# Kernel optimization log

Hardware: AMD Instinct MI355X
Metric: run time of the kernel (lower is better)

## Reference

```python
import jax, jax.numpy as jnp
import numpy as np

D = 1024; DI = 2048; HS = 16; PS = DI // HS; NS = 64; KC = 4; CHUNK = 64
HA = 16; HKV = 4; PA = D // HA; MLP_MULT = 4; ROPE_BASE = 10000.0
B_SZ = 2; L_SEQ = 2048


def rms_norm(x):
    eps = jnp.asarray(jnp.finfo(x.dtype).eps, x.dtype)
    return x * jax.lax.rsqrt(jnp.mean(jnp.square(x), axis=-1, keepdims=True) + eps)


def silu(x):
    return x * jax.nn.sigmoid(x)


def apply_rope(x, cos, sin):
    half = x.shape[-1] // 2
    x1, x2 = x[..., :half], x[..., half:]
    return jnp.concatenate([x1 * cos + x2 * sin, -x1 * sin + x2 * cos], axis=-1)


def selective_scan(x, A, Bm, Cm, dt, chunk):
    # x: [B,L,H,P], Bm/Cm: [B,L,H,N], A/dt: [H]. L must be a multiple of chunk.
    Bb, L, H, P = x.shape
    N = Bm.shape[-1]
    decay = jnp.exp(A * dt)  # [H]
    nc = L // chunk
    xp = x.reshape(Bb, nc, chunk, H, P).transpose(0, 1, 3, 2, 4)   # [B,nc,H,cs,P]
    Bp = Bm.reshape(Bb, nc, chunk, H, N).transpose(0, 1, 3, 2, 4)  # [B,nc,H,cs,N]
    Cp = Cm.reshape(Bb, nc, chunk, H, N).transpose(0, 1, 3, 2, 4)
    x_dt = xp * dt[None, None, :, None, None]
    idx = jnp.arange(chunk)
    diff = idx[:, None] - idx[None, :]
    # intra-chunk causal decay matrix L_mat: [H,cs,cs]
    Lm = jnp.where(diff >= 0, decay[:, None, None] ** jnp.maximum(diff, 0), 0.0)
    CB = jnp.einsum('bchqn,bchkn->bchqk', Cp, Bp)
    y_diag = jnp.einsum('bchqk,bchkp->bchqp', CB * Lm[None, None], x_dt)
    # per-chunk states
    decay_rev = decay[:, None] ** (chunk - 1 - idx)[None, :]  # [H,cs]
    states = jnp.einsum('bchtn,bchtp->bchnp', Bp * decay_rev[None, None, :, :, None], x_dt)
    # inter-chunk propagation
    ci = jnp.arange(nc)
    shift = ci[:, None] - ci[None, :] - 1
    cdec = decay ** chunk
    M = jnp.where(shift >= 0, cdec[:, None, None] ** jnp.maximum(shift, 0), 0.0)  # [H,nc,nc]
    h_carry = jnp.einsum('hij,bjhnp->bihnp', M, states)
    decay_out = decay[:, None] ** (idx + 1)[None, :]  # [H,cs]
    y_off = jnp.einsum('bchtn,bchnp->bchtp', Cp, h_carry) * decay_out[None, None, :, :, None]
    y = (y_diag + y_off).transpose(0, 1, 3, 2, 4).reshape(Bb, L, H, P)
    return y


def mlp(n, fc_w, proj_w):
    h = jax.nn.relu(n @ fc_w)
    return jnp.square(h) @ proj_w


def setup_inputs() -> dict:
    key = jax.random.key(0)
    ks = jax.random.split(key, 24)
    w = lambda k, shp, s=0.02: jax.random.normal(k, shp, jnp.float32) * s
    dt_init = jax.random.uniform(ks[0], (HS,), jnp.float32, 0.001, 0.1)
    dt_bias = dt_init + jnp.log(-jnp.expm1(-dt_init))  # inverse softplus
    return {
        'x': jax.random.normal(ks[1], (B_SZ, L_SEQ, D), jnp.float32),
        'in_proj_w': w(ks[2], (D, 2 * DI)),
        'conv_w': w(ks[3], (DI, KC), 0.2),
        'conv_b': jnp.zeros((DI,), jnp.float32),
        'B_proj_w': w(ks[4], (D, HS * NS)),
        'C_proj_w': w(ks[5], (D, HS * NS)),
        'dt_bias': dt_bias,
        'A_log': jnp.log(jnp.arange(1, HS + 1, dtype=jnp.float32)),
        'D_param': jnp.ones((HS,), jnp.float32),
        'out_proj_w': w(ks[6], (DI, D)),
        'resid_mix_m': jnp.stack([jnp.ones(D), jnp.zeros(D)]).astype(jnp.float32),
        'mamba_scale': jnp.ones((D,), jnp.float32),
        'm_fc_w': w(ks[7], (D, MLP_MULT * D)),
        'm_proj_w': w(ks[8], (MLP_MULT * D, D)),
        'm_mlp_scale': jnp.ones((D,), jnp.float32),
        'resid_mix_a': jnp.stack([jnp.ones(D), jnp.zeros(D)]).astype(jnp.float32),
        'q_w': w(ks[9], (D, D)),
        'k_w': w(ks[10], (D, HKV * PA)),
        'v_w': w(ks[11], (D, HKV * PA)),
        'o_w': w(ks[12], (D, D)),
        'q_gain': jnp.full((HA,), 1.0, jnp.float32),
        'attn_scale': jnp.ones((D,), jnp.float32),
        'a_fc_w': w(ks[13], (D, MLP_MULT * D)),
        'a_proj_w': w(ks[14], (MLP_MULT * D, D)),
        'a_mlp_scale': jnp.ones((D,), jnp.float32),
    }


def reference(x, in_proj_w, conv_w, conv_b, B_proj_w, C_proj_w, dt_bias, A_log, D_param, out_proj_w, resid_mix_m, mamba_scale, m_fc_w, m_proj_w, m_mlp_scale, resid_mix_a, q_w, k_w, v_w, o_w, q_gain, attn_scale, a_fc_w, a_proj_w, a_mlp_scale):
    Bb, L, _ = x.shape
    x0 = x
    # ---- Mamba block ----
    xm = resid_mix_m[0][None, None] * x + resid_mix_m[1][None, None] * x0
    n = rms_norm(xm)
    vg = n @ in_proj_w
    value, gate = vg[..., :DI], vg[..., DI:]
    v_t = value.transpose(0, 2, 1)  # [B, DI, L]
    v_conv = jax.lax.conv_general_dilated(
        v_t, conv_w[:, None, :], (1,), [(KC - 1, 0)],
        feature_group_count=DI, dimension_numbers=('NCH', 'OIH', 'NCH')) + conv_b[None, :, None]
    value = silu(v_conv).transpose(0, 2, 1).reshape(Bb, L, HS, PS)
    Bm = (xm @ B_proj_w).reshape(Bb, L, HS, NS)  # B/C use pre-norm (mixed) input
    Cm = (xm @ C_proj_w).reshape(Bb, L, HS, NS)
    dt = jax.nn.softplus(dt_bias)
    A = -jnp.exp(A_log)
    y = selective_scan(value, A, Bm, Cm, dt, CHUNK)
    y = y + D_param[None, None, :, None] * value
    y = (y.reshape(Bb, L, DI) * silu(gate)) @ out_proj_w
    xm = xm + mamba_scale[None, None] * y
    xm = xm + m_mlp_scale[None, None] * mlp(rms_norm(xm), m_fc_w, m_proj_w)
    # ---- Attention block ----
    xa = resid_mix_a[0][None, None] * xm + resid_mix_a[1][None, None] * x0
    n = rms_norm(xa)
    q = (n @ q_w).reshape(Bb, L, HA, PA).transpose(0, 2, 1, 3)
    k = (n @ k_w).reshape(Bb, L, HKV, PA).transpose(0, 2, 1, 3)
    v = (n @ v_w).reshape(Bb, L, HKV, PA).transpose(0, 2, 1, 3)
    q = rms_norm(q); k = rms_norm(k)
    inv_freq = 1.0 / (ROPE_BASE ** (jnp.arange(0, PA, 2, dtype=jnp.float32) / PA))
    f = jnp.outer(jnp.arange(L, dtype=jnp.float32), inv_freq)
    cos, sin = jnp.cos(f)[None, None], jnp.sin(f)[None, None]
    q = apply_rope(q, cos, sin) * q_gain[None, :, None, None]
    k = apply_rope(k, cos, sin)
    G = HA // HKV
    k = jnp.repeat(k, G, axis=1); v = jnp.repeat(v, G, axis=1)
    s = jnp.einsum('bhqd,bhkd->bhqk', q, k) / np.float32(np.sqrt(PA))
    mask = jnp.tril(jnp.ones((L, L), bool))
    s = jnp.where(mask[None, None], s, jnp.asarray(-jnp.inf, s.dtype))
    att = jax.nn.softmax(s, axis=-1)
    y = jnp.einsum('bhqk,bhkd->bhqd', att, v).transpose(0, 2, 1, 3).reshape(Bb, L, D)
    xa = xa + attn_scale[None, None] * (y @ o_w)
    xa = xa + a_mlp_scale[None, None] * mlp(rms_norm(xa), a_fc_w, a_proj_w)
    return xa
```

## Files before the change

kernel.cpp:

```cpp
#include <hip/hip_runtime.h>
#include <hip/hip_bf16.h>
#include <math.h>

#define D_ 1024
#define DI_ 2048
#define HS_ 16
#define PS_ 128
#define NS_ 64
#define HA_ 16
#define HKV_ 4
#define PA_ 64
#define B_ 2
#define L_ 2048
#define NT_ 4096
#define NC_ 32
#define RMS_EPS_ 1.1920929e-7f

typedef __attribute__((ext_vector_type(8))) short short8;
typedef __attribute__((ext_vector_type(4))) float f32x4;

#define GLOAD_LDS16(gp, lp)                                                        \
  __builtin_amdgcn_global_load_lds(                                               \
      (const __attribute__((address_space(1))) unsigned int*)(gp),                \
      (__attribute__((address_space(3))) unsigned int*)(lp), 16, 0, 0)

__global__ __launch_bounds__(256) void transpose_cvt(
    const float* __restrict__ W, __hip_bfloat16* __restrict__ Wt, int K, int N, int ldw) {
  __shared__ float t[32][33];
  int n0 = blockIdx.x * 32, k0 = blockIdx.y * 32;
  int tx = threadIdx.x & 31, ty = threadIdx.x >> 5;
#pragma unroll
  for (int i = 0; i < 4; i++)
    t[ty + i * 8][tx] = W[(size_t)(k0 + ty + i * 8) * ldw + n0 + tx];
  __syncthreads();
#pragma unroll
  for (int i = 0; i < 4; i++)
    Wt[(size_t)(n0 + ty + i * 8) * K + k0 + tx] = __float2bfloat16(t[tx][ty + i * 8]);
}

template<int BN>
__global__ __launch_bounds__(256) void gemm_bf16_t(
    const unsigned short* __restrict__ A, const unsigned short* __restrict__ Wt,
    float* __restrict__ Cf, __hip_bfloat16* __restrict__ Cb,
    const float* __restrict__ baseb, const float* __restrict__ scale,
    int N, int K, int mode) {
  constexpr int nWc = BN / 64;
  constexpr int nWr = 4 / nWc;
  constexpr int MF  = 8 / nWr;
  __shared__ unsigned short As[2][128 * 64];
  __shared__ unsigned short Bs[2][BN * 64];
  int bm = blockIdx.y * 128, bn = blockIdx.x * BN;
  int tid = threadIdx.x;
  int w = tid >> 6, l = tid & 63;
  int wr = w / nWc, wc = w % nWc;
  int l15 = l & 15, lg = l >> 4;
  f32x4 acc[MF][4];
#pragma unroll
  for (int i = 0; i < MF; i++)
#pragma unroll
    for (int j = 0; j < 4; j++) acc[i][j] = (f32x4){0.f, 0.f, 0.f, 0.f};
  int r_ = tid >> 3;
  int s_ = tid & 7;

  auto STAGE = [&](int k0, int nb) {
#pragma unroll
    for (int i = 0; i < 4; i++) {
      int r = i * 32 + r_;
      int kq = s_ ^ (r & 7);
      GLOAD_LDS16(A + (size_t)(bm + r) * K + k0 + kq * 8, &As[nb][r * 64 + s_ * 8]);
    }
#pragma unroll
    for (int i = 0; i < BN / 32; i++) {
      int r = i * 32 + r_;
      int kq = s_ ^ (r & 7);
      GLOAD_LDS16(Wt + (size_t)(bn + r) * K + k0 + kq * 8, &Bs[nb][r * 64 + s_ * 8]);
    }
  };

  STAGE(0, 0);
  __syncthreads();
  int cur = 0;
  for (int k0 = 0; k0 < K; k0 += 64) {
    if (k0 + 64 < K) STAGE(k0 + 64, cur ^ 1);
#pragma unroll
    for (int h = 0; h < 2; h++) {
      short8 af[MF], bfr[4];
#pragma unroll
      for (int i = 0; i < MF; i++) {
        int row = wr * (16 * MF) + i * 16 + l15;
        int c = h * 4 + lg;
        af[i] = *(const short8*)&As[cur][row * 64 + ((c ^ (row & 7)) << 3)];
      }
#pragma unroll
      for (int j = 0; j < 4; j++) {
        int row = wc * 64 + j * 16 + l15;
        int c = h * 4 + lg;
        bfr[j] = *(const short8*)&Bs[cur][row * 64 + ((c ^ (row & 7)) << 3)];
      }
#pragma unroll
      for (int i = 0; i < MF; i++)
#pragma unroll
        for (int j = 0; j < 4; j++)
          acc[i][j] = __builtin_amdgcn_mfma_f32_16x16x32_bf16(af[i], bfr[j], acc[i][j], 0, 0, 0);
    }
    __syncthreads();
    cur ^= 1;
  }
  int rb = lg * 4, cb2 = l15;
#pragma unroll
  for (int i = 0; i < MF; i++)
#pragma unroll
    for (int j = 0; j < 4; j++) {
      int gr = bm + wr * (16 * MF) + i * 16 + rb;
      int gc = bn + wc * 64 + j * 16 + cb2;
#pragma unroll
      for (int reg = 0; reg < 4; reg++) {
        float v = acc[i][j][reg];
        size_t idx = (size_t)(gr + reg) * N + gc;
        if (mode == 0) {
          Cf[idx] = v;
        } else if (mode == 1) {
          v = fmaxf(v, 0.f);
          Cb[idx] = __float2bfloat16(v * v);
        } else if (mode == 2) {
          Cb[idx] = __float2bfloat16(v);
        } else {
          Cf[idx] = baseb[idx] + scale[gc] * v;
        }
      }
    }
}

__global__ __launch_bounds__(256) void mix_rms_kernel(
    const float* __restrict__ a, const float* __restrict__ b2,
    const float* __restrict__ mix, float* __restrict__ xout,
    __hip_bfloat16* __restrict__ nbf, __hip_bfloat16* __restrict__ rawbf) {
  int row = blockIdx.x;
  size_t base = (size_t)row * D_;
  float v[4]; float ss = 0.f;
#pragma unroll
  for (int i = 0; i < 4; i++) {
    int d = threadIdx.x + i * 256;
    float val = mix[d] * a[base + d] + mix[D_ + d] * b2[base + d];
    v[i] = val; ss += val * val;
  }
  for (int o = 32; o > 0; o >>= 1) ss += __shfl_down(ss, o, 64);
  __shared__ float red[4];
  if ((threadIdx.x & 63) == 0) red[threadIdx.x >> 6] = ss;
  __syncthreads();
  float inv = rsqrtf((red[0] + red[1] + red[2] + red[3]) * (1.f / D_) + RMS_EPS_);
#pragma unroll
  for (int i = 0; i < 4; i++) {
    int d = threadIdx.x + i * 256;
    xout[base + d] = v[i];
    nbf[base + d] = __float2bfloat16(v[i] * inv);
    if (rawbf) rawbf[base + d] = __float2bfloat16(v[i]);
  }
}

__global__ __launch_bounds__(256) void rms_kernel(
    const float* __restrict__ a, __hip_bfloat16* __restrict__ nbf) {
  int row = blockIdx.x;
  size_t base = (size_t)row * D_;
  float v[4]; float ss = 0.f;
#pragma unroll
  for (int i = 0; i < 4; i++) {
    int d = threadIdx.x + i * 256;
    float val = a[base + d];
    v[i] = val; ss += val * val;
  }
  for (int o = 32; o > 0; o >>= 1) ss += __shfl_down(ss, o, 64);
  __shared__ float red[4];
  if ((threadIdx.x & 63) == 0) red[threadIdx.x >> 6] = ss;
  __syncthreads();
  float inv = rsqrtf((red[0] + red[1] + red[2] + red[3]) * (1.f / D_) + RMS_EPS_);
#pragma unroll
  for (int i = 0; i < 4; i++) {
    int d = threadIdx.x + i * 256;
    nbf[base + d] = __float2bfloat16(v[i] * inv);
  }
}

__global__ __launch_bounds__(256) void conv_silu_kernel(
    const __hip_bfloat16* __restrict__ vg, const float* __restrict__ cw,
    const float* __restrict__ cb, float* __restrict__ xv) {
  int idx = blockIdx.x * 256 + threadIdx.x;
  int c = idx & (DI_ - 1);
  int bl = idx >> 11;
  int l = bl & (L_ - 1);
  float acc = cb[c];
  float w0 = cw[c * 4 + 0], w1 = cw[c * 4 + 1], w2 = cw[c * 4 + 2], w3 = cw[c * 4 + 3];
  size_t rb = (size_t)bl * 4096 + c;
  if (l >= 3) acc += __bfloat162float(vg[rb - (size_t)3 * 4096]) * w0;
  if (l >= 2) acc += __bfloat162float(vg[rb - (size_t)2 * 4096]) * w1;
  if (l >= 1) acc += __bfloat162float(vg[rb - (size_t)1 * 4096]) * w2;
  acc += __bfloat162float(vg[rb]) * w3;
  xv[idx] = acc / (1.f + __expf(-acc));
}

__global__ __launch_bounds__(256) void scanA1_kernel(
    const float* __restrict__ xv, const __hip_bfloat16* __restrict__ BCm,
    const float* __restrict__ dt_bias, const float* __restrict__ A_log,
    float* __restrict__ st) {
  __shared__ __align__(16) float sm[4096 + 8192];
  float* Bs = sm;
  float* Xs = sm + 4096;
  int blk = blockIdx.x;
  int c = blk & 31, h = (blk >> 5) & 15, b = blk >> 9;
  float dt = log1pf(__expf(dt_bias[h]));
  float adt = -__expf(A_log[h]) * dt;
  int tid = threadIdx.x;
  int l0 = c * 64;
  size_t rB = ((size_t)(b * L_ + l0)) * 2048 + h * NS_;
#pragma unroll
  for (int i = 0; i < 16; i++) {
    int e = tid + i * 256;
    int t = e >> 6, n = e & 63;
    Bs[t * 64 + n] = __bfloat162float(BCm[rB + (size_t)t * 2048 + n]);
  }
  size_t rX = ((size_t)(b * L_ + l0)) * DI_ + h * PS_;
#pragma unroll
  for (int i = 0; i < 32; i++) {
    int e = tid + i * 256;
    int t = e >> 7, p = e & 127;
    Xs[t * 128 + p] = xv[rX + (size_t)t * DI_ + p];
  }
  __syncthreads();
  int pg = tid & 31;
  int ng = (tid >> 5) << 3;
  float acc[8][4];
#pragma unroll
  for (int nn = 0; nn < 8; nn++)
#pragma unroll
    for (int i = 0; i < 4; i++) acc[nn][i] = 0.f;
  for (int t = 0; t < 64; t++) {
    float dr = __expf(adt * (float)(63 - t));
    float4 x4 = *(const float4*)&Xs[t * 128 + pg * 4];
    float xd0 = x4.x * dr, xd1 = x4.y * dr, xd2 = x4.z * dr, xd3 = x4.w * dr;
#pragma unroll
    for (int nn = 0; nn < 8; nn++) {
      float bv = Bs[t * 64 + ng + nn];
      acc[nn][0] += bv * xd0; acc[nn][1] += bv * xd1;
      acc[nn][2] += bv * xd2; acc[nn][3] += bv * xd3;
    }
  }
  size_t sb = ((size_t)((b * HS_ + h) * NC_ + c)) * (NS_ * PS_);
#pragma unroll
  for (int nn = 0; nn < 8; nn++) {
    *(float4*)&st[sb + (size_t)(ng + nn) * PS_ + pg * 4] =
        make_float4(acc[nn][0] * dt, acc[nn][1] * dt, acc[nn][2] * dt, acc[nn][3] * dt);
  }
}

__global__ __launch_bounds__(256) void scanA2_kernel(
    const float* __restrict__ xv, const __hip_bfloat16* __restrict__ BCm,
    const float* __restrict__ dt_bias,
    const float* __restrict__ A_log, const float* __restrict__ D_param,
    float* __restrict__ y) {
  __shared__ __align__(16) float sm[4160 + 8192];
  float* Cb = sm;
  float* Bs = sm + 4160;
  float* Xs = sm + 4160;
  int blk = blockIdx.x;
  int c = blk & 31, h = (blk >> 5) & 15, b = blk >> 9;
  float dt = log1pf(__expf(dt_bias[h]));
  float adt = -__expf(A_log[h]) * dt;
  float Dp = D_param[h];
  int tid = threadIdx.x;
  int l0 = c * 64;
  size_t rB = ((size_t)(b * L_ + l0)) * 2048 + h * NS_;
#pragma unroll
  for (int i = 0; i < 16; i++) {
    int e = tid + i * 256;
    int t = e >> 6, n = e & 63;
    Bs[t * 64 + n] = __bfloat162float(BCm[rB + (size_t)t * 2048 + n]);
    Cb[t * 65 + n] = __bfloat162float(BCm[rB + 1024 + (size_t)t * 2048 + n]);
  }
  __syncthreads();
  int q = tid >> 2;
  int kb = (tid & 3) << 4;
  float cbl[16];
#pragma unroll
  for (int kk = 0; kk < 16; kk++) {
    int k = kb + kk;
    float a = 0.f;
    if (k <= q) {
      for (int n = 0; n < 64; n++) a += Cb[q * 65 + n] * Bs[k * 64 + n];
      a *= __expf(adt * (float)(q - k));
    }
    cbl[kk] = a;
  }
  __syncthreads();
#pragma unroll
  for (int kk = 0; kk < 16; kk++) Cb[q * 65 + kb + kk] = cbl[kk];
  size_t rX = ((size_t)(b * L_ + l0)) * DI_ + h * PS_;
#pragma unroll
  for (int i = 0; i < 32; i++) {
    int e = tid + i * 256;
    int t = e >> 7, p = e & 127;
    Xs[t * 128 + p] = xv[rX + (size_t)t * DI_ + p];
  }
  __syncthreads();
  int pg = tid & 31;
  int qg = (tid >> 5) << 3;
  float acc[8][4];
#pragma unroll
  for (int qq = 0; qq < 8; qq++)
#pragma unroll
    for (int i = 0; i < 4; i++) acc[qq][i] = 0.f;
  for (int k = 0; k < 64; k++) {
    float4 x4 = *(const float4*)&Xs[k * 128 + pg * 4];
#pragma unroll
    for (int qq = 0; qq < 8; qq++) {
      float s = Cb[(qg + qq) * 65 + k];
      acc[qq][0] += s * x4.x; acc[qq][1] += s * x4.y;
      acc[qq][2] += s * x4.z; acc[qq][3] += s * x4.w;
    }
  }
#pragma unroll
  for (int qq = 0; qq < 8; qq++) {
    int qr = qg + qq;
    float4 xq = *(const float4*)&Xs[qr * 128 + pg * 4];
    size_t yo = ((size_t)(b * L_ + l0 + qr)) * DI_ + h * PS_ + pg * 4;
    *(float4*)&y[yo] = make_float4(acc[qq][0] * dt + Dp * xq.x,
                                   acc[qq][1] * dt + Dp * xq.y,
                                   acc[qq][2] * dt + Dp * xq.z,
                                   acc[qq][3] * dt + Dp * xq.w);
  }
}

__global__ __launch_bounds__(256) void scanB1_kernel(
    float* __restrict__ st, const float* __restrict__ dt_bias,
    const float* __restrict__ A_log) {
  int slice = blockIdx.x & 3;
  int h = (blockIdx.x >> 2) & 15, b = blockIdx.x >> 6;
  float dt = log1pf(__expf(dt_bias[h]));
  float adt = -__expf(A_log[h]) * dt;
  float cdec = __expf(adt * 64.f);
  size_t base = ((size_t)(b * HS_ + h)) * NC_ * (NS_ * PS_) + slice * 2048 + threadIdx.x;
  float hreg[8];
#pragma unroll
  for (int j = 0; j < 8; j++) hreg[j] = 0.f;
  for (int c = 0; c < NC_; c++) {
    size_t o = base + (size_t)c * (NS_ * PS_);
#pragma unroll
    for (int j = 0; j < 8; j++) {
      float tmp = st[o + (size_t)j * 256];
      st[o + (size_t)j * 256] = hreg[j];
      hreg[j] = cdec * hreg[j] + tmp;
    }
  }
}

__global__ __launch_bounds__(256) void scanB2_kernel(
    const __hip_bfloat16* __restrict__ BCm, const float* __restrict__ st,
    const __hip_bfloat16* __restrict__ vg, const float* __restrict__ dt_bias,
    const float* __restrict__ A_log, const float* __restrict__ y,
    __hip_bfloat16* __restrict__ yout) {
  __shared__ float Cs[64 * 64];
  __shared__ __align__(16) float Hs[64 * 128];
  int blk = blockIdx.x;
  int c = blk & 31, h = (blk >> 5) & 15, b = blk >> 9;
  float dt = log1pf(__expf(dt_bias[h]));
  float adt = -__expf(A_log[h]) * dt;
  int tid = threadIdx.x;
  int l0 = c * 64;
  size_t rC = ((size_t)(b * L_ + l0)) * 2048 + 1024 + h * NS_;
#pragma unroll
  for (int i = 0; i < 16; i++) {
    int e = tid + i * 256;
    int t = e >> 6, n = e & 63;
    Cs[t * 64 + n] = __bfloat162float(BCm[rC + (size_t)t * 2048 + n]);
  }
  size_t sb = ((size_t)((b * HS_ + h) * NC_ + c)) * (NS_ * PS_);
#pragma unroll
  for (int i = 0; i < 32; i++) {
    int e = tid + i * 256;
    Hs[e] = st[sb + e];
  }
  __syncthreads();
  int pg = tid & 31;
  int tg = (tid >> 5) << 3;
  float acc[8][4];
#pragma unroll
  for (int tt = 0; tt < 8; tt++)
#pragma unroll
    for (int i = 0; i < 4; i++) acc[tt][i] = 0.f;
  for (int n = 0; n < 64; n++) {
    float4 h4 = *(const float4*)&Hs[n * 128 + pg * 4];
#pragma unroll
    for (int tt = 0; tt < 8; tt++) {
      float cv = Cs[(tg + tt) * 64 + n];
      acc[tt][0] += cv * h4.x; acc[tt][1] += cv * h4.y;
      acc[tt][2] += cv * h4.z; acc[tt][3] += cv * h4.w;
    }
  }
#pragma unroll
  for (int tt = 0; tt < 8; tt++) {
    int t = tg + tt;
    float dout = __expf(adt * (float)(t + 1));
    size_t row = (size_t)(b * L_ + l0 + t);
#pragma unroll
    for (int i = 0; i < 4; i++) {
      int p = pg * 4 + i;
      float g = __bfloat162float(vg[row * 4096 + 2048 + h * PS_ + p]);
      float yv = y[row * DI_ + h * PS_ + p] + acc[tt][i] * dout;
      yout[row * DI_ + h * PS_ + p] = __float2bfloat16(yv * (g / (1.f + __expf(-g))));
    }
  }
}

__global__ void rope_fill_kernel(float* __restrict__ cosb, float* __restrict__ sinb) {
  int idx = blockIdx.x * 256 + threadIdx.x;
  int i = idx & 31, l = idx >> 5;
  float inv = __expf(-(2.0f * (float)i / (float)PA_) * logf(10000.0f));
  float ang = (float)l * inv;
  cosb[idx] = cosf(ang);
  sinb[idx] = sinf(ang);
}

__global__ __launch_bounds__(256) void qknorm_rope_bf16_kernel(
    const float* __restrict__ src, int srcstride, int srcofs,
    __hip_bfloat16* __restrict__ dst, int nh,
    const float* __restrict__ cosb, const float* __restrict__ sinb,
    const float* __restrict__ gain) {
  int row = blockIdx.x * 4 + (threadIdx.x >> 6);
  int lane = threadIdx.x & 63;
  int h = row % nh;
  int tok = row / nh;
  int l = tok & (L_ - 1);
  float v = src[(size_t)tok * srcstride + srcofs + h * 64 + lane];
  float ss = v * v;
  for (int o = 32; o > 0; o >>= 1) ss += __shfl_xor(ss, o, 64);
  v *= rsqrtf(ss * (1.f / PA_) + RMS_EPS_);
  float partner = __shfl_xor(v, 32, 64);
  int i = lane & 31;
  float cth = cosb[l * 32 + i], sth = sinb[l * 32 + i];
  float out = (lane < 32) ? (v * cth + partner * sth) : (v * cth - partner * sth);
  if (gain) out *= gain[h];
  dst[(size_t)tok * (nh * 64) + h * 64 + lane] = __float2bfloat16(out);
}

__global__ __launch_bounds__(256) void attn_mfma_kernel(
    const unsigned short* __restrict__ qb, const unsigned short* __restrict__ kb,
    const unsigned short* __restrict__ vt, __hip_bfloat16* __restrict__ ao) {
  __shared__ unsigned short Ks[64][72];
  __shared__ unsigned short Vs[64][72];
  __shared__ unsigned short Psm[4][16][72];
  int blk = blockIdx.x;
  int qi = blk & 15;
  int h  = (blk >> 4) & 15;
  int b  = blk >> 8;
  int hk = h >> 2;
  int tid = threadIdx.x;
  int w = tid >> 6, l = tid & 63;
  int l15 = l & 15, lg = l >> 4;

  for (int pass = 0; pass < 2; pass++) {
    int qt = pass ? (31 - qi) : qi;
    int q0 = qt * 64;
    int qw = q0 + w * 16;
    short8 qf[2];
    {
      size_t qrow = ((size_t)(b * L_ + qw + l15)) * (HA_ * PA_) + h * PA_;
      qf[0] = *(const short8*)&qb[qrow + lg * 8];
      qf[1] = *(const short8*)&qb[qrow + 32 + lg * 8];
    }
    f32x4 o_acc[4];
#pragma unroll
    for (int db = 0; db < 4; db++) o_acc[db] = (f32x4){0.f, 0.f, 0.f, 0.f};
    float mrow[4] = {-3.0e38f, -3.0e38f, -3.0e38f, -3.0e38f};
    float lsum[4] = {0.f, 0.f, 0.f, 0.f};
    int nkt = qt + 1;
    for (int kt = 0; kt < nkt; kt++) {
      int k0 = kt * 64;
      __syncthreads();
#pragma unroll
      for (int i = 0; i < 2; i++) {
        int e = tid + i * 256;
        int r = e >> 3, s = e & 7;
        *(short8*)&Ks[r][s * 8] =
            *(const short8*)&kb[((size_t)(b * L_ + k0 + r)) * (HKV_ * PA_) + hk * PA_ + s * 8];
        *(short8*)&Vs[r][s * 8] =
            *(const short8*)&vt[((size_t)((b * HKV_ + hk) * PA_ + r)) * L_ + k0 + s * 8];
      }
      __syncthreads();
      f32x4 s_acc[4];
#pragma unroll
      for (int kb2 = 0; kb2 < 4; kb2++) {
        short8 b0 = *(const short8*)&Ks[kb2 * 16 + l15][lg * 8];
        short8 b1 = *(const short8*)&Ks[kb2 * 16 + l15][32 + lg * 8];
        f32x4 s = (f32x4){0.f, 0.f, 0.f, 0.f};
        s = __builtin_amdgcn_mfma_f32_16x16x32_bf16(qf[0], b0, s, 0, 0, 0);
        s = __builtin_amdgcn_mfma_f32_16x16x32_bf16(qf[1], b1, s, 0, 0, 0);
        s_acc[kb2] = s;
      }
      bool diag = (kt == qt);
#pragma unroll
      for (int reg = 0; reg < 4; reg++) {
        float sc[4];
        float tm = -3.0e38f;
#pragma unroll
        for (int kb2 = 0; kb2 < 4; kb2++) {
          float s = s_acc[kb2][reg] * 0.125f;
          if (diag) {
            int key = k0 + kb2 * 16 + l15;
            int qg = qw + lg * 4 + reg;
            if (key > qg) s = -3.0e38f;
          }
          sc[kb2] = s;
          tm = fmaxf(tm, s);
        }
#pragma unroll
        for (int of = 1; of < 16; of <<= 1) tm = fmaxf(tm, __shfl_xor(tm, of, 64));
        float mn = fmaxf(mrow[reg], tm);
        float corr = __expf(mrow[reg] - mn);
        mrow[reg] = mn;
        float rs = 0.f;
        int prow = lg * 4 + reg;
#pragma unroll
        for (int kb2 = 0; kb2 < 4; kb2++) {
          float p = __expf(sc[kb2] - mn);
          rs += p;
          __hip_bfloat16 hv = __float2bfloat16(p);
          Psm[w][prow][kb2 * 16 + l15] = *(unsigned short*)&hv;
        }
#pragma unroll
        for (int of = 1; of < 16; of <<= 1) rs += __shfl_xor(rs, of, 64);
        lsum[reg] = lsum[reg] * corr + rs;
#pragma unroll
        for (int db = 0; db < 4; db++) o_acc[db][reg] *= corr;
      }
      __syncthreads();
#pragma unroll
      for (int ks = 0; ks < 2; ks++) {
        short8 pa = *(const short8*)&Psm[w][l15][ks * 32 + lg * 8];
#pragma unroll
        for (int db = 0; db < 4; db++) {
          short8 vb8 = *(const short8*)&Vs[db * 16 + l15][ks * 32 + lg * 8];
          o_acc[db] = __builtin_amdgcn_mfma_f32_16x16x32_bf16(pa, vb8, o_acc[db], 0, 0, 0);
        }
      }
    }
#pragma unroll
    for (int reg = 0; reg < 4; reg++) {
      float invl = 1.0f / lsum[reg];
      size_t row = (size_t)(b * L_ + qw + lg * 4 + reg);
#pragma unroll
      for (int db = 0; db < 4; db++)
        ao[row * D_ + h * PA_ + db * 16 + l15] = __float2bfloat16(o_acc[db][reg] * invl);
    }
  }
}

extern "C" void kernel_launch(void* const* d_in, const int* in_sizes, int n_in,
                              void* d_out, int out_size, void* d_ws, size_t ws_size,
                              hipStream_t stream) {
  (void)in_sizes; (void)n_in; (void)out_size; (void)ws_size;
  const float* x           = (const float*)d_in[0];
  const float* in_proj_w   = (const float*)d_in[1];
  const float* conv_w      = (const float*)d_in[2];
  const float* conv_b      = (const float*)d_in[3];
  const float* B_proj_w    = (const float*)d_in[4];
  const float* C_proj_w    = (const float*)d_in[5];
  const float* dt_bias     = (const float*)d_in[6];
  const float* A_log       = (const float*)d_in[7];
  const float* D_param     = (const float*)d_in[8];
  const float* out_proj_w  = (const float*)d_in[9];
  const float* resid_mix_m = (const float*)d_in[10];
  const float* mamba_scale = (const float*)d_in[11];
  const float* m_fc_w      = (const float*)d_in[12];
  const float* m_proj_w    = (const float*)d_in[13];
  const float* m_mlp_scale = (const float*)d_in[14];
  const float* resid_mix_a = (const float*)d_in[15];
  const float* q_w         = (const float*)d_in[16];
  const float* k_w         = (const float*)d_in[17];
  const float* v_w         = (const float*)d_in[18];
  const float* o_w         = (const float*)d_in[19];
  const float* q_gain      = (const float*)d_in[20];
  const float* attn_scale  = (const float*)d_in[21];
  const float* a_fc_w      = (const float*)d_in[22];
  const float* a_proj_w    = (const float*)d_in[23];
  const float* a_mlp_scale = (const float*)d_in[24];
  float* ws  = (float*)d_ws;
  float* out = (float*)d_out;

  float* xm    = ws;
  float* vgR   = ws + 4194304;
  float* xvR   = ws + 12582912;
  float* stR   = ws + 20971520;
  float* nbR   = ws + 29360128;
  float* xmbR  = ws + 31457280;
  float* BCR   = ws + 33554432;
  float* WtR   = ws + 37748736;
  float* cosb  = ws + 51642368;
  float* sinb  = cosb + 65536;

  __hip_bfloat16* vg  = (__hip_bfloat16*)vgR;
  float*          qkvf = vgR;
  float*          xv  = xvR;
  float*          st  = stR;
  __hip_bfloat16* hb  = (__hip_bfloat16*)stR;
  __hip_bfloat16* nbb = (__hip_bfloat16*)nbR;
  __hip_bfloat16* xmb = (__hip_bfloat16*)xmbR;
  __hip_bfloat16* ybb = (__hip_bfloat16*)nbR;
  __hip_bfloat16* BCm = (__hip_bfloat16*)BCR;
  __hip_bfloat16* qbb = (__hip_bfloat16*)xvR;
  __hip_bfloat16* kbb = (__hip_bfloat16*)(xvR + 2097152);
  __hip_bfloat16* vtb = (__hip_bfloat16*)(xvR + 2621440);
  __hip_bfloat16* aob = (__hip_bfloat16*)(xvR + 3145728);

  __hip_bfloat16* Wt = (__hip_bfloat16*)WtR;
  size_t o_in  = 0;
  size_t o_B   = o_in  + (size_t)4096 * 1024;
  size_t o_out = o_B   + (size_t)2048 * 1024;
  size_t o_mfc = o_out + (size_t)1024 * 2048;
  size_t o_mpj = o_mfc + (size_t)4096 * 1024;
  size_t o_qkv = o_mpj + (size_t)1024 * 4096;
  size_t o_o   = o_qkv + (size_t)1536 * 1024;
  size_t o_afc = o_o   + (size_t)1024 * 1024;
  size_t o_apj = o_afc + (size_t)4096 * 1024;

#define TCVT(Wp, off, K, N) \
  transpose_cvt<<<dim3((N) / 32, (K) / 32), 256, 0, stream>>>((Wp), Wt + (off), (K), (N), (N))
  TCVT(in_proj_w,  o_in,  1024, 4096);
  TCVT(B_proj_w,   o_B,   1024, 1024);
  TCVT(C_proj_w,   o_B + (size_t)1024 * 1024, 1024, 1024);
  TCVT(out_proj_w, o_out, 2048, 1024);
  TCVT(m_fc_w,     o_mfc, 1024, 4096);
  TCVT(m_proj_w,   o_mpj, 4096, 1024);
  TCVT(q_w,        o_qkv, 1024, 1024);
  TCVT(k_w,        o_qkv + (size_t)1024 * 1024, 1024, 256);
  TCVT(v_w,        o_qkv + (size_t)1280 * 1024, 1024, 256);
  TCVT(o_w,        o_o,   1024, 1024);
  TCVT(a_fc_w,     o_afc, 1024, 4096);
  TCVT(a_proj_w,   o_apj, 4096, 1024);
#undef TCVT

#define GEMM(BN, Abuf, Woff, Cfp, Cbp, basep, scalep, N, K, mode) \
  gemm_bf16_t<BN><<<dim3((N) / (BN), NT_ / 128), 256, 0, stream>>>( \
      (const unsigned short*)(Abuf), (const unsigned short*)(Wt + (Woff)), \
      (Cfp), (Cbp), (basep), (scalep), (N), (K), (mode))

  mix_rms_kernel<<<NT_, 256, 0, stream>>>(x, x, resid_mix_m, xm, nbb, xmb);
  GEMM(128, nbb, o_in, (float*)0, vg, (const float*)0, (const float*)0, 4096, 1024, 2);
  GEMM(128, xmb, o_B, (float*)0, BCm, (const float*)0, (const float*)0, 2048, 1024, 2);
  conv_silu_kernel<<<NT_ * DI_ / 256, 256, 0, stream>>>(vg, conv_w, conv_b, xv);
  scanA1_kernel<<<B_ * HS_ * NC_, 256, 0, stream>>>(xv, BCm, dt_bias, A_log, st);
  scanA2_kernel<<<B_ * HS_ * NC_, 256, 0, stream>>>(xv, BCm, dt_bias, A_log, D_param, xv);
  scanB1_kernel<<<B_ * HS_ * 4, 256, 0, stream>>>(st, dt_bias, A_log);
  scanB2_kernel<<<B_ * HS_ * NC_, 256, 0, stream>>>(BCm, st, vg, dt_bias, A_log, xv, ybb);
  GEMM(64, ybb, o_out, xm, (__hip_bfloat16*)0, xm, mamba_scale, 1024, 2048, 3);
  rms_kernel<<<NT_, 256, 0, stream>>>(xm, nbb);
  GEMM(128, nbb, o_mfc, (float*)0, hb, (const float*)0, (const float*)0, 4096, 1024, 1);
  GEMM(64, hb, o_mpj, xm, (__hip_bfloat16*)0, xm, m_mlp_scale, 1024, 4096, 3);
  mix_rms_kernel<<<NT_, 256, 0, stream>>>(xm, x, resid_mix_a, xm, nbb, (__hip_bfloat16*)0);
  GEMM(64, nbb, o_qkv, qkvf, (__hip_bfloat16*)0, (const float*)0, (const float*)0, 1536, 1024, 0);
  rope_fill_kernel<<<L_ * 32 / 256, 256, 0, stream>>>(cosb, sinb);
  qknorm_rope_bf16_kernel<<<NT_ * HA_ / 4, 256, 0, stream>>>(qkvf, 1536, 0, qbb, HA_, cosb, sinb, q_gain);
  qknorm_rope_bf16_kernel<<<NT_ * HKV_ / 4, 256, 0, stream>>>(qkvf, 1536, 1024, kbb, HKV_, cosb, sinb, (const float*)0);
  transpose_cvt<<<dim3(256 / 32, 2048 / 32), 256, 0, stream>>>(qkvf + 1280, vtb, 2048, 256, 1536);
  transpose_cvt<<<dim3(256 / 32, 2048 / 32), 256, 0, stream>>>(qkvf + (size_t)L_ * 1536 + 1280, vtb + (size_t)256 * L_, 2048, 256, 1536);
  attn_mfma_kernel<<<B_ * HA_ * 16, 256, 0, stream>>>(
      (const unsigned short*)qbb, (const unsigned short*)kbb, (const unsigned short*)vtb, aob);
  GEMM(64, aob, o_o, xm, (__hip_bfloat16*)0, xm, attn_scale, 1024, 1024, 3);
  rms_kernel<<<NT_, 256, 0, stream>>>(xm, nbb);
  GEMM(128, nbb, o_afc, (float*)0, hb, (const float*)0, (const float*)0, 4096, 1024, 1);
  GEMM(64, hb, o_apj, out, (__hip_bfloat16*)0, xm, a_mlp_scale, 1024, 4096, 3);
#undef GEMM
}
```

Baseline: 766.0 us.

## Use static softmax max bound and register-prefetch K/V tiles in attention

Since q and k are RMS-normalized and q is scaled by q_gain, scores are bounded by 8*|q_gain|, so the online-softmax running max, rescaling and per-tile shuffle reductions are replaced by a fixed offset, with the row sum reduced once at the end. Next K/V tiles are prefetched into registers while the current tile is computed. One block-wide barrier is replaced by a wave-local LDS wait, which holds because each wave reads only its own P rows. The bound relies on normalization, and very negative scores could underflow, which costs some accuracy.

After: 711.3 us. 1.08x faster.

```diff
diff --git a/kernel.cpp b/kernel.cpp
--- a/kernel.cpp
+++ b/kernel.cpp
@@ -443,7 +443,8 @@
 
 __global__ __launch_bounds__(256) void attn_mfma_kernel(
     const unsigned short* __restrict__ qb, const unsigned short* __restrict__ kb,
-    const unsigned short* __restrict__ vt, __hip_bfloat16* __restrict__ ao) {
+    const unsigned short* __restrict__ vt, const float* __restrict__ qgain,
+    __hip_bfloat16* __restrict__ ao) {
   __shared__ unsigned short Ks[64][72];
   __shared__ unsigned short Vs[64][72];
   __shared__ unsigned short Psm[4][16][72];
@@ -455,6 +456,10 @@
   int tid = threadIdx.x;
   int w = tid >> 6, l = tid & 63;
   int l15 = l & 15, lg = l >> 4;
+  int r0 = tid >> 3, s0 = tid & 7;
+  float mstat = 8.0f * fabsf(qgain[h]);
+  const unsigned short* kbase = kb + (size_t)b * L_ * (HKV_ * PA_) + hk * PA_ + s0 * 8;
+  const unsigned short* vbase = vt + ((size_t)(b * HKV_ + hk) * PA_) * L_ + s0 * 8;
 
   for (int pass = 0; pass < 2; pass++) {
     int qt = pass ? (31 - qi) : qi;
@@ -469,20 +474,25 @@
     f32x4 o_acc[4];
 #pragma unroll
     for (int db = 0; db < 4; db++) o_acc[db] = (f32x4){0.f, 0.f, 0.f, 0.f};
-    float mrow[4] = {-3.0e38f, -3.0e38f, -3.0e38f, -3.0e38f};
-    float lsum[4] = {0.f, 0.f, 0.f, 0.f};
+    f32x4 lsum = (f32x4){0.f, 0.f, 0.f, 0.f};
     int nkt = qt + 1;
+    short8 kr0 = *(const short8*)&kbase[(size_t)r0 * (HKV_ * PA_)];
+    short8 kr1 = *(const short8*)&kbase[(size_t)(r0 + 32) * (HKV_ * PA_)];
+    short8 vr0 = *(const short8*)&vbase[(size_t)r0 * L_];
+    short8 vr1 = *(const short8*)&vbase[(size_t)(r0 + 32) * L_];
     for (int kt = 0; kt < nkt; kt++) {
       int k0 = kt * 64;
       __syncthreads();
-#pragma unroll
-      for (int i = 0; i < 2; i++) {
-        int e = tid + i * 256;
-        int r = e >> 3, s = e & 7;
-        *(short8*)&Ks[r][s * 8] =
-            *(const short8*)&kb[((size_t)(b * L_ + k0 + r)) * (HKV_ * PA_) + hk * PA_ + s * 8];
-        *(short8*)&Vs[r][s * 8] =
-            *(const short8*)&vt[((size_t)((b * HKV_ + hk) * PA_ + r)) * L_ + k0 + s * 8];
+      *(short8*)&Ks[r0][s0 * 8] = kr0;
+      *(short8*)&Ks[r0 + 32][s0 * 8] = kr1;
+      *(short8*)&Vs[r0][s0 * 8] = vr0;
+      *(short8*)&Vs[r0 + 32][s0 * 8] = vr1;
+      if (kt + 1 < nkt) {
+        int k1 = k0 + 64;
+        kr0 = *(const short8*)&kbase[(size_t)(k1 + r0) * (HKV_ * PA_)];
+        kr1 = *(const short8*)&kbase[(size_t)(k1 + r0 + 32) * (HKV_ * PA_)];
+        vr0 = *(const short8*)&vbase[(size_t)r0 * L_ + k1];
+        vr1 = *(const short8*)&vbase[(size_t)(r0 + 32) * L_ + k1];
       }
       __syncthreads();
       f32x4 s_acc[4];
@@ -497,41 +507,18 @@
       }
       bool diag = (kt == qt);
 #pragma unroll
-      for (int reg = 0; reg < 4; reg++) {
-        float sc[4];
-        float tm = -3.0e38f;
-#pragma unroll
-        for (int kb2 = 0; kb2 < 4; kb2++) {
-          float s = s_acc[kb2][reg] * 0.125f;
-          if (diag) {
-            int key = k0 + kb2 * 16 + l15;
-            int qg = qw + lg * 4 + reg;
-            if (key > qg) s = -3.0e38f;
-          }
-          sc[kb2] = s;
-          tm = fmaxf(tm, s);
+      for (int kb2 = 0; kb2 < 4; kb2++) {
+        int key = k0 + kb2 * 16 + l15;
+#pragma unroll
+        for (int reg = 0; reg < 4; reg++) {
+          float p = __expf(s_acc[kb2][reg] * 0.125f - mstat);
+          if (diag && key > qw + lg * 4 + reg) p = 0.f;
+          lsum[reg] += p;
+          __hip_bfloat16 hv = __float2bfloat16(p);
+          Psm[w][lg * 4 + reg][kb2 * 16 + l15] = *(unsigned short*)&hv;
         }
-#pragma unroll
-        for (int of = 1; of < 16; of <<= 1) tm = fmaxf(tm, __shfl_xor(tm, of, 64));
-        float mn = fmaxf(mrow[reg], tm);
-        float corr = __expf(mrow[reg] - mn);
-        mrow[reg] = mn;
-        float rs = 0.f;
-        int prow = lg * 4 + reg;
-#pragma unroll
-        for (int kb2 = 0; kb2 < 4; kb2++) {
-          float p = __expf(sc[kb2] - mn);
-          rs += p;
-          __hip_bfloat16 hv = __float2bfloat16(p);
-          Psm[w][prow][kb2 * 16 + l15] = *(unsigned short*)&hv;
-        }
-#pragma unroll
-        for (int of = 1; of < 16; of <<= 1) rs += __shfl_xor(rs, of, 64);
-        lsum[reg] = lsum[reg] * corr + rs;
-#pragma unroll
-        for (int db = 0; db < 4; db++) o_acc[db][reg] *= corr;
       }
-      __syncthreads();
+      asm volatile("s_waitcnt lgkmcnt(0)" ::: "memory");
 #pragma unroll
       for (int ks = 0; ks < 2; ks++) {
         short8 pa = *(const short8*)&Psm[w][l15][ks * 32 + lg * 8];
@@ -541,6 +528,13 @@
           o_acc[db] = __builtin_amdgcn_mfma_f32_16x16x32_bf16(pa, vb8, o_acc[db], 0, 0, 0);
         }
       }
+    }
+#pragma unroll
+    for (int of = 1; of < 16; of <<= 1) {
+      lsum[0] += __shfl_xor(lsum[0], of, 64);
+      lsum[1] += __shfl_xor(lsum[1], of, 64);
+      lsum[2] += __shfl_xor(lsum[2], of, 64);
+      lsum[3] += __shfl_xor(lsum[3], of, 64);
     }
 #pragma unroll
     for (int reg = 0; reg < 4; reg++) {
@@ -662,7 +656,8 @@
   transpose_cvt<<<dim3(256 / 32, 2048 / 32), 256, 0, stream>>>(qkvf + 1280, vtb, 2048, 256, 1536);
   transpose_cvt<<<dim3(256 / 32, 2048 / 32), 256, 0, stream>>>(qkvf + (size_t)L_ * 1536 + 1280, vtb + (size_t)256 * L_, 2048, 256, 1536);
   attn_mfma_kernel<<<B_ * HA_ * 16, 256, 0, stream>>>(
-      (const unsigned short*)qbb, (const unsigned short*)kbb, (const unsigned short*)vtb, aob);
+      (const unsigned short*)qbb, (const unsigned short*)kbb, (const unsigned short*)vtb,
+      q_gain, aob);
   GEMM(64, aob, o_o, xm, (__hip_bfloat16*)0, xm, attn_scale, 1024, 1024, 3);
   rms_kernel<<<NT_, 256, 0, stream>>>(xm, nbb);
   GEMM(128, nbb, o_afc, (float*)0, hb, (const float*)0, (const float*)0, 4096, 1024, 1);
```
